# Kernel optimization log

Hardware: AMD Instinct MI355X
Metric: run time of the kernel (lower is better)

Reference implementation:

```python
import jax, jax.numpy as jnp
import numpy as np

G, DIN, DOUT, R = 8, 1024, 1024, 16
N = 8192
SCALE = 32.0 / 16.0  # alpha / r


def grouped_linear(x, W, mask):
    """Grouped linear: out[n] = x[n] @ W[g[n]].
    x: [N, din], W: [G, din, dout], mask: [N, G] one-hot (float).
    Computed as all-group matmul + select; the fused grouped-GEMM is the
    kernel opportunity this reference baselines."""
    y_all = jnp.einsum('ni,gio->gno', x, W)      # [G, N, dout]
    return jnp.einsum('gno,ng->no', y_all, mask)  # [N, dout]


def setup_inputs() -> dict:
    key = jax.random.key(0)
    k1, k2, k3, k4, k5 = jax.random.split(key, 5)
    x = jax.random.normal(k1, (N, DIN), dtype=jnp.float32)
    x_groups = jnp.sort(jax.random.randint(k2, (N,), 0, G, dtype=jnp.int64))
    W_base = jax.random.normal(k3, (G, DIN, DOUT), dtype=jnp.float32) * 0.02
    W_A = jax.random.normal(k4, (G, DIN, R), dtype=jnp.float32) * 0.02
    # original inits lora_B to zero; use small random values so the LoRA path
    # contributes nonzero signal for correctness testing
    W_B = jax.random.normal(k5, (G, R, DOUT), dtype=jnp.float32) * 0.02
    return {"x": x, "x_groups": x_groups, "W_base": W_base, "W_A": W_A, "W_B": W_B}


def reference(x, x_groups, W_base, W_A, W_B):
    mask = (x_groups[:, None] == jnp.arange(G)).astype(x.dtype)  # [N, G] one-hot
    base = grouped_linear(x, W_base, mask)            # base GroupedLinear
    a = grouped_linear(x, W_A, mask)                  # lora_A (dropout p=0 -> identity)
    adapt = grouped_linear(a, W_B, mask)              # lora_B
    return base + SCALE * adapt
```

## Files before the change

### kernel.cpp

```cpp
#include <hip/hip_runtime.h>
#include <stdint.h>

#define N_TOK 8192
#define DIN   1024
#define DOUT  1024
#define NG    8
#define LSCALE 2.0f
#define WROWS (DOUT + 16)

typedef __attribute__((ext_vector_type(4))) float  float4v;
typedef __attribute__((ext_vector_type(8))) short  short8;
typedef short8  frag_ab;
typedef float4v frag_cd;

__device__ __forceinline__ short f2bf(float f) {
    union { float f; uint32_t u; } v; v.f = f;
    uint32_t r = v.u + 0x7fffu + ((v.u >> 16) & 1u);
    return (short)(r >> 16);
}

__device__ __forceinline__ void load_lds16(const void* g, void* lds) {
    __builtin_amdgcn_global_load_lds(
        (const __attribute__((address_space(1))) uint32_t*)g,
        (__attribute__((address_space(3))) uint32_t*)lds,
        16, 0, 0);
}

#define PREP_GRID 6273

__global__ __launch_bounds__(256) void prep_kernel(
        const float* __restrict__ x, const float* __restrict__ Wb,
        const float* __restrict__ WA, const float* __restrict__ WB,
        const int* __restrict__ groups,
        short* __restrict__ xb, short* __restrict__ WtA,
        short* __restrict__ WBt, int* __restrict__ starts) {
    __shared__ float tile[64][65];
    const int blk = blockIdx.x, t = threadIdx.x;

    if (blk < 4096) {
        size_t idx = (size_t)(blk * 256 + t) * 8;
        const float4v* p = (const float4v*)(x + idx);
        float4v a = p[0], b = p[1];
        short8 o;
        o[0]=f2bf(a[0]); o[1]=f2bf(a[1]); o[2]=f2bf(a[2]); o[3]=f2bf(a[3]);
        o[4]=f2bf(b[0]); o[5]=f2bf(b[1]); o[6]=f2bf(b[2]); o[7]=f2bf(b[3]);
        *(short8*)(xb + idx) = o;
    } else if (blk < 6144) {
        int b = blk - 4096;
        int g = b >> 8, rem = b & 255;
        int n0 = (rem & 15) * 64, k0 = (rem >> 4) * 64;
        const float* Wg = Wb + (size_t)g * DIN * DOUT;
#pragma unroll
        for (int i = 0; i < 4; ++i) {
            int idx = i * 256 + t;
            int r = idx >> 4, c = (idx & 15) * 4;
            float4v v = *(const float4v*)(Wg + (size_t)(k0 + r) * DOUT + n0 + c);
            tile[r][c+0]=v[0]; tile[r][c+1]=v[1]; tile[r][c+2]=v[2]; tile[r][c+3]=v[3];
        }
        __syncthreads();
        short* Wtg = WtA + (size_t)g * WROWS * DIN;
#pragma unroll
        for (int i = 0; i < 2; ++i) {
            int idx = i * 256 + t;
            int n = idx >> 3, c8 = (idx & 7) * 8;
            short8 o;
#pragma unroll
            for (int j = 0; j < 8; ++j) o[j] = f2bf(tile[c8 + j][n]);
            *(short8*)(Wtg + (size_t)(n0 + n) * DIN + k0 + c8) = o;
        }
    } else if (blk < 6176) {
        int idx = (blk - 6144) * 256 + t;
        int g = idx >> 10, n = idx & 1023;
        const float* src = WB + (size_t)g * 16 * DOUT + n;
        short8 o0, o1;
#pragma unroll
        for (int r = 0; r < 8; ++r) o0[r] = f2bf(src[(size_t)r * DOUT]);
#pragma unroll
        for (int r = 0; r < 8; ++r) o1[r] = f2bf(src[(size_t)(r + 8) * DOUT]);
        short* dst = WBt + (size_t)idx * 32;
        *(short8*)dst        = o0;
        *(short8*)(dst + 8)  = o1;
        *(short8*)(dst + 16) = (short8)0;
        *(short8*)(dst + 24) = (short8)0;
    } else if (blk < 6240) {
        int tid = (blk - 6176) * 256 + t;
        size_t o = (size_t)tid * 8;
        int g  = (int)(o >> 14);
        int rm = (int)(o & 16383);
        int r  = rm >> 10;
        int k0 = rm & 1023;
        const float* src = WA + (size_t)g * DIN * 16 + r;
        short8 ov;
#pragma unroll
        for (int j = 0; j < 8; ++j) ov[j] = f2bf(src[(size_t)(k0 + j) * 16]);
        *(short8*)(WtA + ((size_t)g * WROWS + DOUT + r) * DIN + k0) = ov;
    } else {
        int i = (blk - 6240) * 256 + t;
        if (i > N_TOK) return;
        int cur  = (i < N_TOK) ? groups[i] : NG;
        int prev = (i == 0) ? -1 : groups[i - 1];
        for (int g = prev + 1; g <= cur; ++g) starts[g] = i;
    }
}

#define BM 128
#define BN 128
#define BK 128
#define NKT (DIN / BK)

__global__ __launch_bounds__(256, 2)
void gemm_grouped(const short* __restrict__ xb,
                  const short* __restrict__ WtA,
                  const short* __restrict__ WBt,
                  const int*   __restrict__ starts,
                  float* __restrict__ out) {
    __shared__ short As[BM * BK];
    __shared__ short Bs[BN * BK];

    const int t    = threadIdx.x;
    const int lane = t & 63;
    const int wid  = t >> 6;
    const int L        = blockIdx.x;
    const int row_tile = (L & 7) * 8 + (L >> 6);
    const int col_tile = (L >> 3) & 7;
    const int col0 = col_tile * BN;
    const int row0 = row_tile * BM;
    const int wr   = (wid >> 1) * 64;
    const int wc   = (wid & 1) * 64;
    const int m16  = lane & 15;
    const int q    = lane >> 4;
    const bool do_a = (wid & 1) == 0;
    const int phase = ((L >> 3) & 1) * 4;

    int gbeg = 0;
    while (starts[gbeg + 1] <= row0) ++gbeg;

    for (int g = gbeg; g < NG && starts[g] < row0 + BM; ++g) {
        const int rlo = starts[g]     > row0      ? starts[g]     : row0;
        const int rhi = starts[g + 1] < row0 + BM ? starts[g + 1] : row0 + BM;
        if (rlo >= rhi) continue;

        const short* wg = WtA + (size_t)g * WROWS * DIN;

        frag_cd acc[4][4];
        frag_cd acc_a[4];
#pragma unroll
        for (int i = 0; i < 4; ++i) {
#pragma unroll
            for (int j = 0; j < 4; ++j) { frag_cd z = {0.f,0.f,0.f,0.f}; acc[i][j] = z; }
            frag_cd z = {0.f,0.f,0.f,0.f}; acc_a[i] = z;
        }

        __syncthreads();

        for (int kt_ii = 0; kt_ii < NKT; ++kt_ii) {
            const int kt = ((kt_ii + phase) & (NKT - 1)) * BK;

#pragma unroll
            for (int i = 0; i < 8; ++i) {
                int Lc = i * 256 + t;
                int r  = Lc >> 4;
                int c8 = (Lc & 15) ^ (r & 7);
                load_lds16(xb + (size_t)(row0 + r) * DIN + kt + c8 * 8,
                           &As[(i * 256 + wid * 64) * 8]);
            }
#pragma unroll
            for (int i = 0; i < 8; ++i) {
                int Lc = i * 256 + t;
                int r  = Lc >> 4;
                int c8 = (Lc & 15) ^ (r & 7);
                load_lds16(wg + (size_t)(col0 + r) * DIN + kt + c8 * 8,
                           &Bs[(i * 256 + wid * 64) * 8]);
            }
            frag_ab ba[4];
            if (do_a) {
                const short* tp = wg + (size_t)(DOUT + m16) * DIN + kt + q * 8;
#pragma unroll
                for (int j = 0; j < 4; ++j) ba[j] = *(const frag_ab*)(tp + j * 32);
            }
            __syncthreads();

#pragma unroll
            for (int kk = 0; kk < BK; kk += 32) {
                frag_ab af[4], bf[4];
                const int ch = (kk >> 3) + q;
#pragma unroll
                for (int mi = 0; mi < 4; ++mi) {
                    int rr = wr + mi * 16 + m16;
                    af[mi] = *(const frag_ab*)&As[rr * BK + ((ch ^ (rr & 7)) << 3)];
                }
#pragma unroll
                for (int ni = 0; ni < 4; ++ni) {
                    int cc = wc + ni * 16 + m16;
                    bf[ni] = *(const frag_ab*)&Bs[cc * BK + ((ch ^ (cc & 7)) << 3)];
                }
#pragma unroll
                for (int mi = 0; mi < 4; ++mi)
#pragma unroll
                    for (int ni = 0; ni < 4; ++ni)
                        acc[mi][ni] = __builtin_amdgcn_mfma_f32_16x16x32_bf16(
                            af[mi], bf[ni], acc[mi][ni], 0, 0, 0);
                if (do_a) {
#pragma unroll
                    for (int mi = 0; mi < 4; ++mi)
                        acc_a[mi] = __builtin_amdgcn_mfma_f32_16x16x32_bf16(
                            af[mi], ba[kk >> 5], acc_a[mi], 0, 0, 0);
                }
            }
            __syncthreads();
        }

        short* a_lds = As;
        {
            int row = t >> 1, cz = 16 + (t & 1) * 8;
            *(short8*)&a_lds[row * 40 + cz] = (short8)0;
        }
        if (do_a) {
#pragma unroll
            for (int mi = 0; mi < 4; ++mi)
#pragma unroll
                for (int r = 0; r < 4; ++r) {
                    int row = wr + mi * 16 + q * 4 + r;
                    a_lds[row * 40 + m16] = f2bf(acc_a[mi][r] * LSCALE);
                }
        }
        __syncthreads();
        {
            frag_ab af[4], bfw[4];
#pragma unroll
            for (int mi = 0; mi < 4; ++mi)
                af[mi] = *(const frag_ab*)&a_lds[(wr + mi * 16 + m16) * 40 + q * 8];
#pragma unroll
            for (int ni = 0; ni < 4; ++ni)
                bfw[ni] = *(const frag_ab*)&WBt[((size_t)g * DOUT + col0 + wc + ni * 16 + m16) * 32 + q * 8];
#pragma unroll
            for (int mi = 0; mi < 4; ++mi)
#pragma unroll
                for (int ni = 0; ni < 4; ++ni)
                    acc[mi][ni] = __builtin_amdgcn_mfma_f32_16x16x32_bf16(
                        af[mi], bfw[ni], acc[mi][ni], 0, 0, 0);
        }

#pragma unroll
        for (int mi = 0; mi < 4; ++mi)
#pragma unroll
            for (int r = 0; r < 4; ++r) {
                int grow = row0 + wr + mi * 16 + q * 4 + r;
                if (grow >= rlo && grow < rhi) {
                    float* orow = out + (size_t)grow * DOUT + col0 + wc + m16;
#pragma unroll
                    for (int ni = 0; ni < 4; ++ni) orow[ni * 16] = acc[mi][ni][r];
                }
            }
    }
}

extern "C" void kernel_launch(void* const* d_in, const int* in_sizes, int n_in,
                              void* d_out, int out_size, void* d_ws, size_t ws_size,
                              hipStream_t stream) {
    const float* x      = (const float*)d_in[0];
    const int*   groups = (const int*)d_in[1];
    const float* Wb     = (const float*)d_in[2];
    const float* WA     = (const float*)d_in[3];
    const float* WB     = (const float*)d_in[4];
    float* out = (float*)d_out;

    char* ws = (char*)d_ws;
    int*   starts = (int*)ws;
    short* xb     = (short*)(ws + 1024);
    short* WtA    = (short*)(ws + 1024 + (size_t)16 * 1024 * 1024);
    short* WBt    = (short*)(ws + 1024 + (size_t)33 * 1024 * 1024);

    hipLaunchKernelGGL(prep_kernel, dim3(PREP_GRID), dim3(256), 0, stream,
                       x, Wb, WA, WB, groups, xb, WtA, WBt, starts);
    hipLaunchKernelGGL(gemm_grouped, dim3(512), dim3(256), 0, stream,
                       xb, WtA, WBt, starts, out);
}
```

Measured before the change: 148.5 us.

## Fold LoRA A·B product into base weights during prep, drop LoRA path from GEMM

The prep kernel now computes W_base + scale·(W_A @ W_B) per group tile in fp32 and writes one merged bf16 weight matrix. The grouped GEMM then runs a single plain matmul per group, with no extra LoRA-A MFMAs, no LDS round trip for the rank-16 intermediate, and no second small GEMM. The cost is a rank-16 outer-product accumulation in the prep transpose blocks. Rounding also changes, since the low-rank update is added before bf16 conversion rather than applied as a separate product.

```diff
diff --git a/kernel.cpp b/kernel.cpp
--- a/kernel.cpp
+++ b/kernel.cpp
@@ -6,7 +6,6 @@
 #define DOUT  1024
 #define NG    8
 #define LSCALE 2.0f
-#define WROWS (DOUT + 16)
 
 typedef __attribute__((ext_vector_type(4))) float  float4v;
 typedef __attribute__((ext_vector_type(8))) short  short8;
@@ -26,15 +25,17 @@
         16, 0, 0);
 }
 
-#define PREP_GRID 6273
+#define PREP_GRID 6177
 
 __global__ __launch_bounds__(256) void prep_kernel(
         const float* __restrict__ x, const float* __restrict__ Wb,
         const float* __restrict__ WA, const float* __restrict__ WB,
         const int* __restrict__ groups,
-        short* __restrict__ xb, short* __restrict__ WtA,
-        short* __restrict__ WBt, int* __restrict__ starts) {
+        short* __restrict__ xb, short* __restrict__ Wt,
+        int* __restrict__ starts) {
     __shared__ float tile[64][65];
+    __shared__ float At[64][17];
+    __shared__ float Bt[16][64];
     const int blk = blockIdx.x, t = threadIdx.x;
 
     if (blk < 4096) {
@@ -57,45 +58,37 @@
             float4v v = *(const float4v*)(Wg + (size_t)(k0 + r) * DOUT + n0 + c);
             tile[r][c+0]=v[0]; tile[r][c+1]=v[1]; tile[r][c+2]=v[2]; tile[r][c+3]=v[3];
         }
+        {
+            int kk = t >> 2, c = (t & 3) * 4;
+            float4v v = *(const float4v*)(WA + ((size_t)g * DIN + k0 + kk) * 16 + c);
+            At[kk][c+0]=v[0]; At[kk][c+1]=v[1]; At[kk][c+2]=v[2]; At[kk][c+3]=v[3];
+        }
+        {
+            int r = t >> 4, c = (t & 15) * 4;
+            float4v v = *(const float4v*)(WB + ((size_t)g * 16 + r) * DOUT + n0 + c);
+            Bt[r][c+0]=v[0]; Bt[r][c+1]=v[1]; Bt[r][c+2]=v[2]; Bt[r][c+3]=v[3];
+        }
         __syncthreads();
-        short* Wtg = WtA + (size_t)g * WROWS * DIN;
+        short* Wtg = Wt + (size_t)g * DOUT * DIN;
 #pragma unroll
         for (int i = 0; i < 2; ++i) {
             int idx = i * 256 + t;
             int n = idx >> 3, c8 = (idx & 7) * 8;
+            float corr[8] = {0.f,0.f,0.f,0.f,0.f,0.f,0.f,0.f};
+#pragma unroll
+            for (int r = 0; r < 16; ++r) {
+                float bv = Bt[r][n];
+#pragma unroll
+                for (int j = 0; j < 8; ++j) corr[j] += At[c8 + j][r] * bv;
+            }
             short8 o;
 #pragma unroll
-            for (int j = 0; j < 8; ++j) o[j] = f2bf(tile[c8 + j][n]);
+            for (int j = 0; j < 8; ++j)
+                o[j] = f2bf(tile[c8 + j][n] + LSCALE * corr[j]);
             *(short8*)(Wtg + (size_t)(n0 + n) * DIN + k0 + c8) = o;
         }
-    } else if (blk < 6176) {
-        int idx = (blk - 6144) * 256 + t;
-        int g = idx >> 10, n = idx & 1023;
-        const float* src = WB + (size_t)g * 16 * DOUT + n;
-        short8 o0, o1;
-#pragma unroll
-        for (int r = 0; r < 8; ++r) o0[r] = f2bf(src[(size_t)r * DOUT]);
-#pragma unroll
-        for (int r = 0; r < 8; ++r) o1[r] = f2bf(src[(size_t)(r + 8) * DOUT]);
-        short* dst = WBt + (size_t)idx * 32;
-        *(short8*)dst        = o0;
-        *(short8*)(dst + 8)  = o1;
-        *(short8*)(dst + 16) = (short8)0;
-        *(short8*)(dst + 24) = (short8)0;
-    } else if (blk < 6240) {
-        int tid = (blk - 6176) * 256 + t;
-        size_t o = (size_t)tid * 8;
-        int g  = (int)(o >> 14);
-        int rm = (int)(o & 16383);
-        int r  = rm >> 10;
-        int k0 = rm & 1023;
-        const float* src = WA + (size_t)g * DIN * 16 + r;
-        short8 ov;
-#pragma unroll
-        for (int j = 0; j < 8; ++j) ov[j] = f2bf(src[(size_t)(k0 + j) * 16]);
-        *(short8*)(WtA + ((size_t)g * WROWS + DOUT + r) * DIN + k0) = ov;
     } else {
-        int i = (blk - 6240) * 256 + t;
+        int i = (blk - 6144) * 256 + t;
         if (i > N_TOK) return;
         int cur  = (i < N_TOK) ? groups[i] : NG;
         int prev = (i == 0) ? -1 : groups[i - 1];
@@ -110,8 +103,7 @@
 
 __global__ __launch_bounds__(256, 2)
 void gemm_grouped(const short* __restrict__ xb,
-                  const short* __restrict__ WtA,
-                  const short* __restrict__ WBt,
+                  const short* __restrict__ Wt,
                   const int*   __restrict__ starts,
                   float* __restrict__ out) {
     __shared__ short As[BM * BK];
@@ -129,7 +121,6 @@
     const int wc   = (wid & 1) * 64;
     const int m16  = lane & 15;
     const int q    = lane >> 4;
-    const bool do_a = (wid & 1) == 0;
     const int phase = ((L >> 3) & 1) * 4;
 
     int gbeg = 0;
@@ -140,18 +131,13 @@
         const int rhi = starts[g + 1] < row0 + BM ? starts[g + 1] : row0 + BM;
         if (rlo >= rhi) continue;
 
-        const short* wg = WtA + (size_t)g * WROWS * DIN;
+        const short* wg = Wt + (size_t)g * DOUT * DIN;
 
         frag_cd acc[4][4];
-        frag_cd acc_a[4];
-#pragma unroll
-        for (int i = 0; i < 4; ++i) {
+#pragma unroll
+        for (int i = 0; i < 4; ++i)
 #pragma unroll
             for (int j = 0; j < 4; ++j) { frag_cd z = {0.f,0.f,0.f,0.f}; acc[i][j] = z; }
-            frag_cd z = {0.f,0.f,0.f,0.f}; acc_a[i] = z;
-        }
-
-        __syncthreads();
 
         for (int kt_ii = 0; kt_ii < NKT; ++kt_ii) {
             const int kt = ((kt_ii + phase) & (NKT - 1)) * BK;
@@ -172,12 +158,6 @@
                 load_lds16(wg + (size_t)(col0 + r) * DIN + kt + c8 * 8,
                            &Bs[(i * 256 + wid * 64) * 8]);
             }
-            frag_ab ba[4];
-            if (do_a) {
-                const short* tp = wg + (size_t)(DOUT + m16) * DIN + kt + q * 8;
-#pragma unroll
-                for (int j = 0; j < 4; ++j) ba[j] = *(const frag_ab*)(tp + j * 32);
-            }
             __syncthreads();
 
 #pragma unroll
@@ -200,45 +180,8 @@
                     for (int ni = 0; ni < 4; ++ni)
                         acc[mi][ni] = __builtin_amdgcn_mfma_f32_16x16x32_bf16(
                             af[mi], bf[ni], acc[mi][ni], 0, 0, 0);
-                if (do_a) {
-#pragma unroll
-                    for (int mi = 0; mi < 4; ++mi)
-                        acc_a[mi] = __builtin_amdgcn_mfma_f32_16x16x32_bf16(
-                            af[mi], ba[kk >> 5], acc_a[mi], 0, 0, 0);
-                }
             }
             __syncthreads();
-        }
-
-        short* a_lds = As;
-        {
-            int row = t >> 1, cz = 16 + (t & 1) * 8;
-            *(short8*)&a_lds[row * 40 + cz] = (short8)0;
-        }
-        if (do_a) {
-#pragma unroll
-            for (int mi = 0; mi < 4; ++mi)
-#pragma unroll
-                for (int r = 0; r < 4; ++r) {
-                    int row = wr + mi * 16 + q * 4 + r;
-                    a_lds[row * 40 + m16] = f2bf(acc_a[mi][r] * LSCALE);
-                }
-        }
-        __syncthreads();
-        {
-            frag_ab af[4], bfw[4];
-#pragma unroll
-            for (int mi = 0; mi < 4; ++mi)
-                af[mi] = *(const frag_ab*)&a_lds[(wr + mi * 16 + m16) * 40 + q * 8];
-#pragma unroll
-            for (int ni = 0; ni < 4; ++ni)
-                bfw[ni] = *(const frag_ab*)&WBt[((size_t)g * DOUT + col0 + wc + ni * 16 + m16) * 32 + q * 8];
-#pragma unroll
-            for (int mi = 0; mi < 4; ++mi)
-#pragma unroll
-                for (int ni = 0; ni < 4; ++ni)
-                    acc[mi][ni] = __builtin_amdgcn_mfma_f32_16x16x32_bf16(
-                        af[mi], bfw[ni], acc[mi][ni], 0, 0, 0);
         }
 
 #pragma unroll
@@ -268,11 +211,10 @@
     char* ws = (char*)d_ws;
     int*   starts = (int*)ws;
     short* xb     = (short*)(ws + 1024);
-    short* WtA    = (short*)(ws + 1024 + (size_t)16 * 1024 * 1024);
-    short* WBt    = (short*)(ws + 1024 + (size_t)33 * 1024 * 1024);
+    short* Wt     = (short*)(ws + 1024 + (size_t)16 * 1024 * 1024);
 
     hipLaunchKernelGGL(prep_kernel, dim3(PREP_GRID), dim3(256), 0, stream,
-                       x, Wb, WA, WB, groups, xb, WtA, WBt, starts);
+                       x, Wb, WA, WB, groups, xb, Wt, starts);
     hipLaunchKernelGGL(gemm_grouped, dim3(512), dim3(256), 0, stream,
-                       xb, WtA, WBt, starts, out);
-}
+                       xb, Wt, starts, out);
+}
```

After: 153.7 us. 1.03x slower.
